# Kernel optimization log

Measured on AMD Instinct MI355X. Metric: run time of the kernel, lower is better.

Reference implementation:

```python
import jax, jax.numpy as jnp
import numpy as np

B, T, C, HS = 4, 4096, 1024, 128

def setup_inputs() -> dict:
    key = jax.random.key(0)
    kx, kq, kk, kv = jax.random.split(key, 4)
    x = jax.random.normal(kx, (B, T, C), dtype=jnp.float32)
    # bias-free Linear weights, stored as (in, out) so projection is x @ W
    scale = 1.0 / np.sqrt(C)
    Wq = jax.random.normal(kq, (C, HS), dtype=jnp.float32) * scale
    Wk = jax.random.normal(kk, (C, HS), dtype=jnp.float32) * scale
    Wv = jax.random.normal(kv, (C, HS), dtype=jnp.float32) * scale
    return {"x": x, "Wq": Wq, "Wk": Wk, "Wv": Wv}

def reference(x, Wq, Wk, Wv):
    # x: (B,T,C) -> q,k,v: (B,T,HS)
    q = jnp.einsum('btc,ch->bth', x, Wq)
    k = jnp.einsum('btc,ch->bth', x, Wk)
    v = jnp.einsum('btc,ch->bth', x, Wv)
    hs = k.shape[-1]
    # scaled scores (B,T,T) with causal mask
    wei = jnp.einsum('bth,bsh->bts', q, k) * (hs ** -0.5)
    causal = jnp.tril(jnp.ones((q.shape[1], q.shape[1]), dtype=bool))
    wei = jnp.where(causal, wei, -jnp.inf)
    wei = jax.nn.softmax(wei, axis=-1)
    # dropout p=0.0 -> identity
    out = jnp.einsum('bts,bsh->bth', wei, v)
    return out
```

## Files before the change

kernel.cpp:

```cpp
#include <hip/hip_runtime.h>
#include <hip/hip_bf16.h>

typedef __attribute__((ext_vector_type(8))) short short8;
typedef __attribute__((ext_vector_type(4))) short s4v;
typedef __attribute__((ext_vector_type(4))) float f32x4;

#define BATCH 4
#define TLEN 4096
#define CDIM 1024
#define HSD 128
#define MROWS (BATCH*TLEN)

#define QSCALE 0.12751744f

#ifdef __HIP_DEVICE_COMPILE__
  #define MFMA16(a,b,c) __builtin_amdgcn_mfma_f32_16x16x16bf16_1k(a,b,c,0,0,0)
#else
  #define MFMA16(a,b,c) (c)
#endif

__device__ __forceinline__ unsigned short f2bf(float f){
    unsigned u = __builtin_bit_cast(unsigned, f);
    u = (u + 0x7FFFu + ((u >> 16) & 1u)) >> 16;
    return (unsigned short)u;
}
__device__ __forceinline__ unsigned pkbf(float a, float b){
    unsigned ua = (__builtin_bit_cast(unsigned, a) + 0x8000u) >> 16;
    unsigned ub = (__builtin_bit_cast(unsigned, b) + 0x8000u) & 0xFFFF0000u;
    return ua | ub;
}

__global__ void prep_w_k(const float* __restrict__ Wq, const float* __restrict__ Wk,
                         const float* __restrict__ Wv, unsigned short* __restrict__ Wt){
    __shared__ float tile[32][33];
    const int w = blockIdx.z;
    const float* W = (w == 0) ? Wq : ((w == 1) ? Wk : Wv);
    const int c0 = blockIdx.x * 32, h0 = blockIdx.y * 32;
    const int lx = threadIdx.x & 31, ly = threadIdx.x >> 5;
#pragma unroll
    for (int i = 0; i < 4; i++){
        int c = c0 + ly + i * 8;
        tile[ly + i * 8][lx] = W[(size_t)c * HSD + h0 + lx];
    }
    __syncthreads();
#pragma unroll
    for (int i = 0; i < 4; i++){
        int h = h0 + ly + i * 8;
        Wt[((size_t)w * HSD + h) * CDIM + c0 + lx] = f2bf(tile[lx][ly + i * 8]);
    }
}

__device__ __forceinline__ void stage_wb(unsigned short* buf, const unsigned short* g, int tid){
#pragma unroll
    for (int i = 0; i < 3; i++){
        int c = i * 512 + tid;
        int row = c >> 2, kp = c & 3;
        int swz = (row & 3) ^ ((row >> 2) & 3);
        const unsigned short* gp = g + (size_t)row * CDIM + ((kp ^ swz) << 3);
        unsigned short* lp = buf + (c << 3);
        __builtin_amdgcn_global_load_lds((const __attribute__((address_space(1))) void*)gp,
                                         (__attribute__((address_space(3))) void*)lp, 16, 0, 0);
    }
}

__global__ __launch_bounds__(512) void proj_k(const float* __restrict__ x,
                                              const unsigned short* __restrict__ Wt,
                                              unsigned short* __restrict__ Qb,
                                              unsigned short* __restrict__ Kb,
                                              unsigned short* __restrict__ Vt){
    __shared__ unsigned short As[2][64 * 32];
    __shared__ unsigned short Bs[2][384 * 32];

    const int tid = threadIdx.x, lane = tid & 63, wave = tid >> 6;
    const int m = lane & 15, quad = lane >> 4;
    const int wr = wave & 1;
    const int wc = wave >> 1;
    const int rb = blockIdx.x * 64;

    const float* gA = x + (size_t)rb * CDIM;

    const int arow = tid >> 2, ach = tid & 3;
    const int aswz = (arow & 3) ^ ((arow >> 2) & 3);
    const int agc = ach ^ aswz;
    const float* agp = gA + (size_t)arow * CDIM + (agc << 3);

    f32x4 acc[6][2];
#pragma unroll
    for (int i = 0; i < 6; i++)
#pragma unroll
        for (int j = 0; j < 2; j++) acc[i][j] = (f32x4)0.f;

    stage_wb(&Bs[0][0], Wt, tid);
    if (tid < 256){
        float4 a0 = *(const float4*)(agp);
        float4 a1 = *(const float4*)(agp + 4);
        short8 o;
        o[0]=(short)f2bf(a0.x); o[1]=(short)f2bf(a0.y); o[2]=(short)f2bf(a0.z); o[3]=(short)f2bf(a0.w);
        o[4]=(short)f2bf(a1.x); o[5]=(short)f2bf(a1.y); o[6]=(short)f2bf(a1.z); o[7]=(short)f2bf(a1.w);
        *(short8*)&As[0][arow * 32 + (ach << 3)] = o;
    }
    __syncthreads();

    int cur = 0;
    for (int kc = 0; kc < CDIM / 32; ++kc){
        float4 a0n, a1n;
        if (kc + 1 < CDIM / 32){
            stage_wb(&Bs[cur ^ 1][0], Wt + (kc + 1) * 32, tid);
            if (tid < 256){
                a0n = *(const float4*)(agp + (kc + 1) * 32);
                a1n = *(const float4*)(agp + (kc + 1) * 32 + 4);
            }
        }
        {
            short8 aF[6], bF[2];
#pragma unroll
            for (int i = 0; i < 6; i++){
                int ra = wc * 96 + i * 16 + m;
                int sa = (ra & 3) ^ ((ra >> 2) & 3);
                aF[i] = *(const short8*)&Bs[cur][ra * 32 + ((quad ^ sa) << 3)];
            }
#pragma unroll
            for (int j = 0; j < 2; j++){
                int rn = wr * 32 + j * 16 + m;
                int sb = (rn & 3) ^ ((rn >> 2) & 3);
                bF[j] = *(const short8*)&As[cur][rn * 32 + ((quad ^ sb) << 3)];
            }
#pragma unroll
            for (int i = 0; i < 6; i++)
#pragma unroll
                for (int j = 0; j < 2; j++)
                    acc[i][j] = __builtin_amdgcn_mfma_f32_16x16x32_bf16(aF[i], bF[j], acc[i][j], 0, 0, 0);
        }
        if (kc + 1 < CDIM / 32 && tid < 256){
            short8 o;
            o[0]=(short)f2bf(a0n.x); o[1]=(short)f2bf(a0n.y); o[2]=(short)f2bf(a0n.z); o[3]=(short)f2bf(a0n.w);
            o[4]=(short)f2bf(a1n.x); o[5]=(short)f2bf(a1n.y); o[6]=(short)f2bf(a1n.z); o[7]=(short)f2bf(a1n.w);
            *(short8*)&As[cur ^ 1][arow * 32 + (ach << 3)] = o;
        }
        __syncthreads();
        cur ^= 1;
    }

    const int b = rb >> 12;
#pragma unroll
    for (int i = 0; i < 6; i++){
        const int hbase = wc * 96 + i * 16;
        const int type = hbase >> 7;
        const int hp = hbase + quad * 4;
#pragma unroll
        for (int j = 0; j < 2; j++){
            const int t = rb + wr * 32 + j * 16 + m;
            if (type == 0){
                ushort4 v;
                v.x = f2bf(acc[i][j][0] * QSCALE); v.y = f2bf(acc[i][j][1] * QSCALE);
                v.z = f2bf(acc[i][j][2] * QSCALE); v.w = f2bf(acc[i][j][3] * QSCALE);
                *(ushort4*)(Qb + (size_t)t * HSD + hp) = v;
            } else if (type == 1){
                ushort4 v;
                v.x = f2bf(acc[i][j][0]); v.y = f2bf(acc[i][j][1]);
                v.z = f2bf(acc[i][j][2]); v.w = f2bf(acc[i][j][3]);
                *(ushort4*)(Kb + (size_t)t * HSD + (hp - 128)) = v;
            } else {
                const int tt = t & (TLEN - 1);
#pragma unroll
                for (int r = 0; r < 4; r++)
                    Vt[((size_t)b * HSD + (hp - 256 + r)) * TLEN + tt] = f2bf(acc[i][j][r]);
            }
        }
    }
}

__device__ __forceinline__ void stage_k_tile(unsigned short* buf, const unsigned short* g,
                                             int tid){
#pragma unroll
    for (int i = 0; i < 2; i++){
        int slot = i * 512 + tid;
        int row = slot >> 4;
        int ch  = slot & 15;
        const unsigned short* gp = g + row * 128 + ((ch ^ (row & 15)) << 3);
        unsigned short* lp = buf + (slot << 3);
        __builtin_amdgcn_global_load_lds((const __attribute__((address_space(1))) void*)gp,
                                         (__attribute__((address_space(3))) void*)lp, 16, 0, 0);
    }
}
__device__ __forceinline__ void stage_v_tile(unsigned short* buf, const unsigned short* g,
                                             int tid){
#pragma unroll
    for (int i = 0; i < 2; i++){
        int slot = i * 512 + tid;
        int row = slot >> 3;
        int ch  = slot & 7;
        const unsigned short* gp = g + (size_t)row * TLEN + ((ch ^ (row & 7)) << 3);
        unsigned short* lp = buf + (slot << 3);
        __builtin_amdgcn_global_load_lds((const __attribute__((address_space(1))) void*)gp,
                                         (__attribute__((address_space(3))) void*)lp, 16, 0, 0);
    }
}

__global__ __launch_bounds__(512) void attn_k(const unsigned short* __restrict__ Qb,
                       const unsigned short* __restrict__ Kb,
                       const unsigned short* __restrict__ Vts,
                       float* __restrict__ Opart, float* __restrict__ lpart, int seglen){
    __shared__ unsigned short Kt[2][64 * 128];
    __shared__ unsigned short Vs[2][128 * 64];

    const int tid = threadIdx.x, lane = tid & 63, wave = tid >> 6;
    const int m = lane & 15, quad = lane >> 4;
    const int q0 = ((int)gridDim.x - 1 - (int)blockIdx.x) * 128;
    const int seg = blockIdx.y, b = blockIdx.z;
    const int g0 = seg * seglen;
    if (g0 >= q0 + 128) return;
    const int gend = min(g0 + seglen, q0 + 128);
    const int nT = (gend - g0) >> 6;

    const int q0w = q0 + wave * 16;
    const size_t rowg = (size_t)b * TLEN + q0w;

    const unsigned short* kbase = Kb + (size_t)b * TLEN * HSD;
    const unsigned short* vbase = Vts + (size_t)b * HSD * TLEN;

    short8 aQ[4];
#pragma unroll
    for (int kk = 0; kk < 4; kk++)
        aQ[kk] = *(const short8*)(Qb + (rowg + m) * HSD + kk * 32 + quad * 8);

    stage_k_tile(&Kt[0][0], kbase + (size_t)g0 * HSD, tid);
    stage_v_tile(&Vs[0][0], vbase + g0, tid);

    f32x4 accO[8];
#pragma unroll
    for (int i = 0; i < 8; i++) accO[i] = (f32x4)0.f;
    float lp = 0.f;

    asm volatile("s_waitcnt vmcnt(0)" ::: "memory");
#pragma unroll
    for (int kk = 0; kk < 4; kk++){
        f32x4 q_ = __builtin_bit_cast(f32x4, aQ[kk]);
        asm volatile("" : "+v"(q_));
        aQ[kk] = __builtin_bit_cast(short8, q_);
    }

    int cur = 0;
    for (int t = 0; t < nT; ++t){
        const int s0 = g0 + t * 64;
        if (t + 1 < nT){
            stage_k_tile(&Kt[cur ^ 1][0], kbase + (size_t)(s0 + 64) * HSD, tid);
            stage_v_tile(&Vs[cur ^ 1][0], vbase + (s0 + 64), tid);
            asm volatile("s_waitcnt vmcnt(4)" ::: "memory");
        } else {
            asm volatile("s_waitcnt vmcnt(0)" ::: "memory");
        }
        __builtin_amdgcn_s_barrier();
        __builtin_amdgcn_sched_barrier(0);
        if (s0 <= q0w + 15){
            const unsigned short* Ktc = &Kt[cur][0];
            const unsigned short* Vsc = &Vs[cur][0];
            f32x4 S[4];
            __builtin_amdgcn_s_setprio(1);
#pragma unroll
            for (int ns = 0; ns < 4; ns++){
                f32x4 sa = (f32x4)0.f;
#pragma unroll
                for (int kk = 0; kk < 4; kk++){
                    short8 bK = *(const short8*)&Ktc[(ns * 16 + m) * 128 + (((kk * 4 + quad) ^ m) << 3)];
                    sa = __builtin_amdgcn_mfma_f32_16x16x32_bf16(bK, aQ[kk], sa, 0, 0, 0);
                }
                S[ns] = sa;
            }
            __builtin_amdgcn_s_setprio(0);
            if (s0 + 63 > q0w){
                int qg = q0w + m;
#pragma unroll
                for (int ns = 0; ns < 4; ns++){
#pragma unroll
                    for (int r = 0; r < 4; r++){
                        int sg = s0 + ns * 16 + quad * 4 + r;
                        if (sg > qg) S[ns][r] = -1e30f;
                    }
                }
            }
            s4v aP[4];
#pragma unroll
            for (int ns = 0; ns < 4; ns++){
                float p0 = exp2f(S[ns][0]), p1 = exp2f(S[ns][1]);
                float p2 = exp2f(S[ns][2]), p3 = exp2f(S[ns][3]);
                lp += (p0 + p1) + (p2 + p3);
                uint2 u;
                u.x = pkbf(p0, p1);
                u.y = pkbf(p2, p3);
                aP[ns] = __builtin_bit_cast(s4v, u);
            }
            __builtin_amdgcn_s_setprio(1);
#pragma unroll
            for (int sub = 0; sub < 8; sub++){
#pragma unroll
                for (int ns = 0; ns < 4; ns++){
                    s4v bV = *(const s4v*)&Vsc[(sub * 16 + m) * 64 +
                            (((2 * ns + (quad >> 1)) ^ (m & 7)) << 3) + (quad & 1) * 4];
                    accO[sub] = MFMA16(aP[ns], bV, accO[sub]);
                }
            }
            __builtin_amdgcn_s_setprio(0);
        }
        __builtin_amdgcn_sched_barrier(0);
        __builtin_amdgcn_s_barrier();
        cur ^= 1;
    }
    lp += __shfl_xor(lp, 16, 64);
    lp += __shfl_xor(lp, 32, 64);
    if (quad == 0)
        lpart[(size_t)seg * MROWS + rowg + m] = lp;
    float* ob = Opart + (size_t)seg * MROWS * HSD;
#pragma unroll
    for (int sub = 0; sub < 8; sub++)
#pragma unroll
        for (int r = 0; r < 4; r++)
            ob[(rowg + quad * 4 + r) * HSD + sub * 16 + m] = accO[sub][r];
}

__global__ void merge_k(const float* __restrict__ Opart, const float* __restrict__ lpart,
                        float* __restrict__ out, int nseg, int seglen){
    int idx = blockIdx.x * 256 + threadIdx.x;
    int row = idx >> 7;
    int t = row & (TLEN - 1);
    int q0 = t & ~127;
    int nsv = min(nseg, (q0 + 127) / seglen + 1);
    float L = 0.f, o = 0.f;
    for (int s = 0; s < nsv; s++){
        L += lpart[(size_t)s * MROWS + row];
        o += Opart[(size_t)s * MROWS * HSD + idx];
    }
    out[idx] = o / L;
}

extern "C" void kernel_launch(void* const* d_in, const int* in_sizes, int n_in,
                              void* d_out, int out_size, void* d_ws, size_t ws_size,
                              hipStream_t stream) {
    const float* x  = (const float*)d_in[0];
    const float* Wq = (const float*)d_in[1];
    const float* Wk = (const float*)d_in[2];
    const float* Wv = (const float*)d_in[3];
    float* out = (float*)d_out;
    char* w = (char*)d_ws;

    unsigned short* Wt = (unsigned short*)w;
    unsigned short* Qb = (unsigned short*)(w + ((size_t)1u  << 20));
    unsigned short* Kb = (unsigned short*)(w + ((size_t)5u  << 20));
    unsigned short* Vt = (unsigned short*)(w + ((size_t)9u  << 20));
    float* lpart       = (float*)(w + ((size_t)13u << 20));
    float* Opart;
    int nseg;
    const size_t segbytes = (size_t)MROWS * HSD * 4;
    if (ws_size >= ((size_t)14u << 20) + 8 * segbytes){
        nseg = 8;  Opart = (float*)(w + ((size_t)14u << 20));
    } else if (ws_size >= ((size_t)14u << 20) + 4 * segbytes){
        nseg = 4;  Opart = (float*)(w + ((size_t)14u << 20));
    } else {
        nseg = 1;  Opart = out;
    }
    const int seglen = TLEN / nseg;

    prep_w_k<<<dim3(CDIM / 32, HSD / 32, 3), 256, 0, stream>>>(Wq, Wk, Wv, Wt);
    proj_k<<<dim3(MROWS / 64), 512, 0, stream>>>(x, Wt, Qb, Kb, Vt);
    attn_k<<<dim3(TLEN / 128, nseg, BATCH), 512, 0, stream>>>(Qb, Kb, Vt, Opart, lpart, seglen);
    merge_k<<<(MROWS * HSD) / 256, 256, 0, stream>>>(Opart, lpart, out, nseg, seglen);
}
```

Baseline: 200.5 us.

## Shrink attention KV tiles to 32, add 16-way split, restructure projection pipeline

The attention kernel now stages 32-key tiles instead of 64, which halves LDS per block and adds a launch-bounds occupancy hint. It also allows 16 key segments when the workspace is large enough. The projection kernel now has all 512 threads load and convert A in 4-wide chunks, and replaces __syncthreads with explicit vmcnt waits plus s_barrier. The aim is more resident blocks and parallelism, and less causal tail waste. The cost is more loop iterations, more merge work over partial outputs, and possible LDS hazards from the barrier placement changes.

```diff
diff --git a/kernel.cpp b/kernel.cpp
--- a/kernel.cpp
+++ b/kernel.cpp
@@ -79,10 +79,11 @@
 
     const float* gA = x + (size_t)rb * CDIM;
 
-    const int arow = tid >> 2, ach = tid & 3;
-    const int aswz = (arow & 3) ^ ((arow >> 2) & 3);
-    const int agc = ach ^ aswz;
-    const float* agp = gA + (size_t)arow * CDIM + (agc << 3);
+    const int arow = tid >> 3, ach = tid & 7;
+    const int asw = (arow & 3) ^ ((arow >> 2) & 3);
+    const float* agp = gA + (size_t)arow * CDIM + ((((ach >> 1) ^ asw) << 3) + (ach & 1) * 4);
+    unsigned short* asp0 = &As[0][arow * 32 + (ach << 2)];
+    unsigned short* asp1 = &As[1][arow * 32 + (ach << 2)];
 
     f32x4 acc[6][2];
 #pragma unroll
@@ -91,26 +92,26 @@
         for (int j = 0; j < 2; j++) acc[i][j] = (f32x4)0.f;
 
     stage_wb(&Bs[0][0], Wt, tid);
-    if (tid < 256){
+    {
         float4 a0 = *(const float4*)(agp);
-        float4 a1 = *(const float4*)(agp + 4);
-        short8 o;
-        o[0]=(short)f2bf(a0.x); o[1]=(short)f2bf(a0.y); o[2]=(short)f2bf(a0.z); o[3]=(short)f2bf(a0.w);
-        o[4]=(short)f2bf(a1.x); o[5]=(short)f2bf(a1.y); o[6]=(short)f2bf(a1.z); o[7]=(short)f2bf(a1.w);
-        *(short8*)&As[0][arow * 32 + (ach << 3)] = o;
+        ushort4 o;
+        o.x = f2bf(a0.x); o.y = f2bf(a0.y); o.z = f2bf(a0.z); o.w = f2bf(a0.w);
+        *(ushort4*)asp0 = o;
     }
     __syncthreads();
 
     int cur = 0;
     for (int kc = 0; kc < CDIM / 32; ++kc){
-        float4 a0n, a1n;
+        float4 a0n;
         if (kc + 1 < CDIM / 32){
+            a0n = *(const float4*)(agp + (kc + 1) * 32);
             stage_wb(&Bs[cur ^ 1][0], Wt + (kc + 1) * 32, tid);
-            if (tid < 256){
-                a0n = *(const float4*)(agp + (kc + 1) * 32);
-                a1n = *(const float4*)(agp + (kc + 1) * 32 + 4);
-            }
-        }
+            asm volatile("s_waitcnt vmcnt(4)" ::: "memory");
+        } else {
+            asm volatile("s_waitcnt vmcnt(0)" ::: "memory");
+        }
+        __builtin_amdgcn_s_barrier();
+        __builtin_amdgcn_sched_barrier(0);
         {
             short8 aF[6], bF[2];
 #pragma unroll
@@ -131,15 +132,14 @@
                 for (int j = 0; j < 2; j++)
                     acc[i][j] = __builtin_amdgcn_mfma_f32_16x16x32_bf16(aF[i], bF[j], acc[i][j], 0, 0, 0);
         }
-        if (kc + 1 < CDIM / 32 && tid < 256){
-            short8 o;
-            o[0]=(short)f2bf(a0n.x); o[1]=(short)f2bf(a0n.y); o[2]=(short)f2bf(a0n.z); o[3]=(short)f2bf(a0n.w);
-            o[4]=(short)f2bf(a1n.x); o[5]=(short)f2bf(a1n.y); o[6]=(short)f2bf(a1n.z); o[7]=(short)f2bf(a1n.w);
-            *(short8*)&As[cur ^ 1][arow * 32 + (ach << 3)] = o;
-        }
-        __syncthreads();
+        if (kc + 1 < CDIM / 32){
+            ushort4 o;
+            o.x = f2bf(a0n.x); o.y = f2bf(a0n.y); o.z = f2bf(a0n.z); o.w = f2bf(a0n.w);
+            *(ushort4*)((cur == 0) ? asp1 : asp0) = o;
+        }
         cur ^= 1;
     }
+    __builtin_amdgcn_s_barrier();
 
     const int b = rb >> 12;
 #pragma unroll
@@ -172,37 +172,29 @@
 
 __device__ __forceinline__ void stage_k_tile(unsigned short* buf, const unsigned short* g,
                                              int tid){
-#pragma unroll
-    for (int i = 0; i < 2; i++){
-        int slot = i * 512 + tid;
-        int row = slot >> 4;
-        int ch  = slot & 15;
-        const unsigned short* gp = g + row * 128 + ((ch ^ (row & 15)) << 3);
-        unsigned short* lp = buf + (slot << 3);
-        __builtin_amdgcn_global_load_lds((const __attribute__((address_space(1))) void*)gp,
-                                         (__attribute__((address_space(3))) void*)lp, 16, 0, 0);
-    }
+    int row = tid >> 4;
+    int ch  = tid & 15;
+    const unsigned short* gp = g + row * 128 + ((ch ^ (row & 15)) << 3);
+    unsigned short* lp = buf + (tid << 3);
+    __builtin_amdgcn_global_load_lds((const __attribute__((address_space(1))) void*)gp,
+                                     (__attribute__((address_space(3))) void*)lp, 16, 0, 0);
 }
 __device__ __forceinline__ void stage_v_tile(unsigned short* buf, const unsigned short* g,
                                              int tid){
-#pragma unroll
-    for (int i = 0; i < 2; i++){
-        int slot = i * 512 + tid;
-        int row = slot >> 3;
-        int ch  = slot & 7;
-        const unsigned short* gp = g + (size_t)row * TLEN + ((ch ^ (row & 7)) << 3);
-        unsigned short* lp = buf + (slot << 3);
-        __builtin_amdgcn_global_load_lds((const __attribute__((address_space(1))) void*)gp,
-                                         (__attribute__((address_space(3))) void*)lp, 16, 0, 0);
-    }
-}
-
-__global__ __launch_bounds__(512) void attn_k(const unsigned short* __restrict__ Qb,
+    int row = tid >> 2;
+    int ch  = tid & 3;
+    const unsigned short* gp = g + (size_t)row * TLEN + ((ch ^ (row & 3)) << 3);
+    unsigned short* lp = buf + (tid << 3);
+    __builtin_amdgcn_global_load_lds((const __attribute__((address_space(1))) void*)gp,
+                                     (__attribute__((address_space(3))) void*)lp, 16, 0, 0);
+}
+
+__global__ __launch_bounds__(512, 8) void attn_k(const unsigned short* __restrict__ Qb,
                        const unsigned short* __restrict__ Kb,
                        const unsigned short* __restrict__ Vts,
                        float* __restrict__ Opart, float* __restrict__ lpart, int seglen){
-    __shared__ unsigned short Kt[2][64 * 128];
-    __shared__ unsigned short Vs[2][128 * 64];
+    __shared__ unsigned short Kt[2][32 * 128];
+    __shared__ unsigned short Vs[2][128 * 32];
 
     const int tid = threadIdx.x, lane = tid & 63, wave = tid >> 6;
     const int m = lane & 15, quad = lane >> 4;
@@ -211,7 +203,7 @@
     const int g0 = seg * seglen;
     if (g0 >= q0 + 128) return;
     const int gend = min(g0 + seglen, q0 + 128);
-    const int nT = (gend - g0) >> 6;
+    const int nT = (gend - g0) >> 5;
 
     const int q0w = q0 + wave * 16;
     const size_t rowg = (size_t)b * TLEN + q0w;
@@ -242,11 +234,11 @@
 
     int cur = 0;
     for (int t = 0; t < nT; ++t){
-        const int s0 = g0 + t * 64;
+        const int s0 = g0 + t * 32;
         if (t + 1 < nT){
-            stage_k_tile(&Kt[cur ^ 1][0], kbase + (size_t)(s0 + 64) * HSD, tid);
-            stage_v_tile(&Vs[cur ^ 1][0], vbase + (s0 + 64), tid);
-            asm volatile("s_waitcnt vmcnt(4)" ::: "memory");
+            stage_k_tile(&Kt[cur ^ 1][0], kbase + (size_t)(s0 + 32) * HSD, tid);
+            stage_v_tile(&Vs[cur ^ 1][0], vbase + (s0 + 32), tid);
+            asm volatile("s_waitcnt vmcnt(2)" ::: "memory");
         } else {
             asm volatile("s_waitcnt vmcnt(0)" ::: "memory");
         }
@@ -255,10 +247,10 @@
         if (s0 <= q0w + 15){
             const unsigned short* Ktc = &Kt[cur][0];
             const unsigned short* Vsc = &Vs[cur][0];
-            f32x4 S[4];
+            f32x4 S[2];
             __builtin_amdgcn_s_setprio(1);
 #pragma unroll
-            for (int ns = 0; ns < 4; ns++){
+            for (int ns = 0; ns < 2; ns++){
                 f32x4 sa = (f32x4)0.f;
 #pragma unroll
                 for (int kk = 0; kk < 4; kk++){
@@ -268,10 +260,10 @@
                 S[ns] = sa;
             }
             __builtin_amdgcn_s_setprio(0);
-            if (s0 + 63 > q0w){
+            if (s0 + 31 > q0w){
                 int qg = q0w + m;
 #pragma unroll
-                for (int ns = 0; ns < 4; ns++){
+                for (int ns = 0; ns < 2; ns++){
 #pragma unroll
                     for (int r = 0; r < 4; r++){
                         int sg = s0 + ns * 16 + quad * 4 + r;
@@ -279,24 +271,22 @@
                     }
                 }
             }
-            s4v aP[4];
-#pragma unroll
-            for (int ns = 0; ns < 4; ns++){
+            s4v aP[2];
+#pragma unroll
+            for (int ns = 0; ns < 2; ns++){
                 float p0 = exp2f(S[ns][0]), p1 = exp2f(S[ns][1]);
                 float p2 = exp2f(S[ns][2]), p3 = exp2f(S[ns][3]);
                 lp += (p0 + p1) + (p2 + p3);
-                uint2 u;
-                u.x = pkbf(p0, p1);
-                u.y = pkbf(p2, p3);
+                uint2 u; u.x = pkbf(p0, p1); u.y = pkbf(p2, p3);
                 aP[ns] = __builtin_bit_cast(s4v, u);
             }
             __builtin_amdgcn_s_setprio(1);
 #pragma unroll
             for (int sub = 0; sub < 8; sub++){
 #pragma unroll
-                for (int ns = 0; ns < 4; ns++){
-                    s4v bV = *(const s4v*)&Vsc[(sub * 16 + m) * 64 +
-                            (((2 * ns + (quad >> 1)) ^ (m & 7)) << 3) + (quad & 1) * 4];
+                for (int ns = 0; ns < 2; ns++){
+                    s4v bV = *(const s4v*)&Vsc[(sub * 16 + m) * 32 +
+                            (((2 * ns + (quad >> 1)) ^ (m & 3)) << 3) + (quad & 1) * 4];
                     accO[sub] = MFMA16(aP[ns], bV, accO[sub]);
                 }
             }
@@ -351,7 +341,9 @@
     float* Opart;
     int nseg;
     const size_t segbytes = (size_t)MROWS * HSD * 4;
-    if (ws_size >= ((size_t)14u << 20) + 8 * segbytes){
+    if (ws_size >= ((size_t)14u << 20) + 16 * segbytes){
+        nseg = 16; Opart = (float*)(w + ((size_t)14u << 20));
+    } else if (ws_size >= ((size_t)14u << 20) + 8 * segbytes){
         nseg = 8;  Opart = (float*)(w + ((size_t)14u << 20));
     } else if (ws_size >= ((size_t)14u << 20) + 4 * segbytes){
         nseg = 4;  Opart = (float*)(w + ((size_t)14u << 20));
```

New measurement: 313.5 us. 56.4% more time.
